# Optimization experiments

Hardware: AMD Instinct MI355X
Metric: run time of the kernel (lower is better)

The kernel has to match this reference:

```python
import jax, jax.numpy as jnp
import numpy as np

H = 8            # num_heads
WIN = 128        # num_windows (sliding-window half-width)
B, T, C = 2, 4096, 512


def setup_inputs() -> dict:
    key = jax.random.key(0)
    k1, k2, k3 = jax.random.split(key, 3)
    x = jax.random.normal(k1, (B, T, C), dtype=jnp.float32)
    W_qkv = jax.random.normal(k2, (C, 3 * C), dtype=jnp.float32) * (C ** -0.5)
    W_out = jax.random.normal(k3, (C, C), dtype=jnp.float32) * (C ** -0.5)
    b_out = jnp.zeros((C,), dtype=jnp.float32)
    return {"x": x, "W_qkv": W_qkv, "W_out": W_out, "b_out": b_out}


def reference(x, W_qkv, W_out, b_out):
    Bx, Tx, Cx = x.shape
    hd = Cx // H
    scale = hd ** -0.5
    # qkv projection -> [B, T, 3, H, hd]
    qkv = (x @ W_qkv).reshape(Bx, Tx, 3, H, hd)
    q, k, v = qkv[:, :, 0], qkv[:, :, 1], qkv[:, :, 2]  # each [B, T, H, hd]
    # attention scores [B, H, T, T]
    scores = jnp.einsum('bihd,bjhd->bhij', q, k) * scale
    idx = jnp.arange(Tx)
    band = jnp.abs(idx[:, None] - idx[None, :]) <= WIN  # [T, T] bool
    scores = jnp.where(band[None, None], scores, jnp.float32(-jnp.inf))
    attn = jax.nn.softmax(scores, axis=-1)
    # dropout is identity in eval mode (p handled by config; omitted)
    out = jnp.einsum('bhij,bjhd->bihd', attn, v).reshape(Bx, Tx, Cx)
    return out @ W_out + b_out
```

## Files before the change

kernel.cpp:

```cpp
#include <hip/hip_runtime.h>
#include <stdint.h>

typedef unsigned short ushort_t;
typedef __attribute__((ext_vector_type(8))) __bf16 bf16x8;
typedef __attribute__((ext_vector_type(8))) unsigned short ushortx8;
typedef __attribute__((ext_vector_type(4))) float floatx4;
typedef __attribute__((ext_vector_type(4))) unsigned int uint4v;

__device__ inline ushort_t f2bf(float f) {
  union { float f; unsigned u; } v; v.f = f;
  unsigned r = v.u + 0x7FFFu + ((v.u >> 16) & 1u);
  return (ushort_t)(r >> 16);
}

__device__ inline floatx4 mfma16(bf16x8 a, bf16x8 b, floatx4 c) {
  return __builtin_amdgcn_mfma_f32_16x16x32_bf16(a, b, c, 0, 0, 0);
}

__device__ inline void gload_lds16(const ushort_t* g, ushort_t* l) {
  __builtin_amdgcn_global_load_lds((__attribute__((address_space(1))) void*)(void*)(g),
                                   (__attribute__((address_space(3))) void*)(l),
                                   16, 0, 0);
}

__global__ __launch_bounds__(256)
void k_prep(const float* __restrict__ x, ushort_t* __restrict__ xb,
            const float* __restrict__ Wqkv, ushort_t* __restrict__ wqkvT,
            const float* __restrict__ Wout, ushort_t* __restrict__ woutT) {
  int bx = blockIdx.x, tid = threadIdx.x;
  if (bx < 4096) {
    int i = (bx * 256 + tid) * 4;
    float4 v = *(const float4*)(x + i);
    ushort4 o;
    o.x = f2bf(v.x); o.y = f2bf(v.y); o.z = f2bf(v.z); o.w = f2bf(v.w);
    *(ushort4*)(xb + i) = o;
    return;
  }
  __shared__ float tile[32][33];
  const float* src; ushort_t* dst; int N, id;
  if (bx < 4096 + 768) { id = bx - 4096; src = Wqkv; dst = wqkvT; N = 1536; }
  else                 { id = bx - 4864; src = Wout; dst = woutT; N = 512;  }
  int k0 = (id & 15) * 32, n0 = (id >> 4) * 32;
  int c = tid & 31, r0 = tid >> 5;
#pragma unroll
  for (int i = 0; i < 4; ++i) {
    int r = r0 + i * 8;
    tile[r][c] = src[(size_t)(k0 + r) * N + n0 + c];
  }
  __syncthreads();
#pragma unroll
  for (int i = 0; i < 4; ++i) {
    int r = r0 + i * 8;
    dst[(size_t)(n0 + r) * 512 + k0 + c] = f2bf(tile[c][r]);
  }
}

__global__ __launch_bounds__(256)
void k_gemm1(const ushort_t* __restrict__ A, const ushort_t* __restrict__ Bt,
             ushort_t* __restrict__ qd, ushort_t* __restrict__ kd,
             ushort_t* __restrict__ vtd) {
  __shared__ __align__(16) ushort_t smem[17408];
  ushort_t* As = smem;
  ushort_t* Bs = smem + 8192;
  const int tid = threadIdx.x;
  const int w = tid >> 6, l = tid & 63;
  const int lr = l & 15, lq = l >> 4;
  const int m0 = blockIdx.x * 128, n0 = blockIdx.y * 128;
  const int wm = w >> 1, wn = w & 1;

  floatx4 acc[4][4];
#pragma unroll
  for (int i = 0; i < 4; ++i)
#pragma unroll
    for (int j = 0; j < 4; ++j) acc[i][j] = (floatx4)0.0f;

  for (int k0 = 0; k0 < 512; k0 += 64) {
#pragma unroll
    for (int i = 0; i < 8; ++i) {
      int idx = w * 8 + i;
      if (idx < 16) {
        int blk = idx >> 1, half = idx & 1;
        gload_lds16(A + (size_t)(m0 + blk * 16 + lr) * 512 + k0 + half * 32 + lq * 8,
                    &As[blk * 1024 + half * 512]);
      } else {
        int j = idx - 16, blk = j >> 1, half = j & 1;
        gload_lds16(Bt + (size_t)(n0 + blk * 16 + lr) * 512 + k0 + half * 32 + lq * 8,
                    &Bs[blk * 1024 + half * 512]);
      }
    }
    __syncthreads();
#pragma unroll
    for (int half = 0; half < 2; ++half) {
      bf16x8 af[4], bfr[4];
#pragma unroll
      for (int i = 0; i < 4; ++i)
        af[i] = *(const bf16x8*)&As[(wm * 4 + i) * 1024 + half * 512 + l * 8];
#pragma unroll
      for (int j = 0; j < 4; ++j)
        bfr[j] = *(const bf16x8*)&Bs[(wn * 4 + j) * 1024 + half * 512 + l * 8];
#pragma unroll
      for (int i = 0; i < 4; ++i)
#pragma unroll
        for (int j = 0; j < 4; ++j) acc[i][j] = mfma16(af[i], bfr[j], acc[i][j]);
    }
    __syncthreads();
  }

  if (blockIdx.y < 8) {
#pragma unroll
    for (int i = 0; i < 4; ++i)
#pragma unroll
      for (int j = 0; j < 4; ++j) {
        int col = wn * 64 + j * 16 + lr;
#pragma unroll
        for (int r = 0; r < 4; ++r) {
          int row = wm * 64 + i * 16 + lq * 4 + r;
          smem[row * 136 + col] = f2bf(acc[i][j][r]);
        }
      }
    __syncthreads();
#pragma unroll
    for (int p = 0; p < 8; ++p) {
      int row = p * 16 + (tid >> 4), c8 = (tid & 15) * 8;
      ushortx8 vv = *(const ushortx8*)&smem[row * 136 + c8];
      int n = n0 + c8;
      ushort_t* dst = (n >> 9) ? kd : qd;
      int h = (n >> 6) & 7, d = n & 63;
      int m = m0 + row, b = m >> 12, t = m & 4095;
      *(ushortx8*)&dst[(((size_t)(b * 8 + h)) * 4096 + t) * 64 + d] = vv;
    }
  } else {
#pragma unroll
    for (int i = 0; i < 4; ++i)
#pragma unroll
      for (int j = 0; j < 4; ++j) {
        int dcol = wn * 64 + j * 16 + lr;
        int trow = wm * 64 + i * 16 + lq * 4;
        ushort4 pv;
        pv.x = f2bf(acc[i][j][0]); pv.y = f2bf(acc[i][j][1]);
        pv.z = f2bf(acc[i][j][2]); pv.w = f2bf(acc[i][j][3]);
        *(ushort4*)&smem[dcol * 136 + trow] = pv;
      }
    __syncthreads();
#pragma unroll
    for (int p = 0; p < 8; ++p) {
      int row = p * 16 + (tid >> 4), c8 = (tid & 15) * 8;
      ushortx8 vv = *(const ushortx8*)&smem[row * 136 + c8];
      int n = n0 + row, h = (n >> 6) & 7, d = n & 63;
      int m = m0 + c8, b = m >> 12, t = m & 4095;
      *(ushortx8*)&vtd[(((size_t)(b * 8 + h)) * 64 + d) * 4096 + t] = vv;
    }
  }
}

__global__ __launch_bounds__(256)
void k_gemm2(const ushort_t* __restrict__ A, const ushort_t* __restrict__ Bt,
             float* __restrict__ outf, const float* __restrict__ bias) {
  __shared__ __align__(16) char smemc[33792];
  ushort_t* As = (ushort_t*)smemc;
  ushort_t* Bs = (ushort_t*)(smemc + 8192);
  float* Cs = (float*)smemc;
  const int tid = threadIdx.x;
  const int w = tid >> 6, l = tid & 63;
  const int lr = l & 15, lq = l >> 4;
  const int m0 = blockIdx.x * 64, n0 = blockIdx.y * 128;
  const int wm = w >> 1, wn = w & 1;

  floatx4 acc[2][4];
#pragma unroll
  for (int i = 0; i < 2; ++i)
#pragma unroll
    for (int j = 0; j < 4; ++j) acc[i][j] = (floatx4)0.0f;

  for (int k0 = 0; k0 < 512; k0 += 64) {
#pragma unroll
    for (int i = 0; i < 6; ++i) {
      int idx = w * 6 + i;
      if (idx < 8) {
        int blk = idx >> 1, half = idx & 1;
        gload_lds16(A + (size_t)(m0 + blk * 16 + lr) * 512 + k0 + half * 32 + lq * 8,
                    &As[blk * 1024 + half * 512]);
      } else {
        int j = idx - 8, blk = j >> 1, half = j & 1;
        gload_lds16(Bt + (size_t)(n0 + blk * 16 + lr) * 512 + k0 + half * 32 + lq * 8,
                    &Bs[blk * 1024 + half * 512]);
      }
    }
    __syncthreads();
#pragma unroll
    for (int half = 0; half < 2; ++half) {
      bf16x8 af[2], bfr[4];
#pragma unroll
      for (int i = 0; i < 2; ++i)
        af[i] = *(const bf16x8*)&As[(wm * 2 + i) * 1024 + half * 512 + l * 8];
#pragma unroll
      for (int j = 0; j < 4; ++j)
        bfr[j] = *(const bf16x8*)&Bs[(wn * 4 + j) * 1024 + half * 512 + l * 8];
#pragma unroll
      for (int i = 0; i < 2; ++i)
#pragma unroll
        for (int j = 0; j < 4; ++j) acc[i][j] = mfma16(af[i], bfr[j], acc[i][j]);
    }
    __syncthreads();
  }

#pragma unroll
  for (int i = 0; i < 2; ++i)
#pragma unroll
    for (int j = 0; j < 4; ++j) {
      int col = wn * 64 + j * 16 + lr;
      float bv = bias[n0 + col];
#pragma unroll
      for (int r = 0; r < 4; ++r) {
        int row = wm * 32 + i * 16 + lq * 4 + r;
        Cs[row * 132 + col] = acc[i][j][r] + bv;
      }
    }
  __syncthreads();
#pragma unroll
  for (int p = 0; p < 4; ++p) {
    int row = p * 16 + (tid >> 4), c = (tid & 15) * 8;
    float4 v0 = *(const float4*)&Cs[row * 132 + c];
    float4 v1 = *(const float4*)&Cs[row * 132 + c + 4];
    float* op = &outf[(size_t)(m0 + row) * 512 + n0 + c];
    *(float4*)op = v0;
    *(float4*)(op + 4) = v1;
  }
}

__global__ __launch_bounds__(256)
void k_attn(const ushort_t* __restrict__ qa, const ushort_t* __restrict__ ka,
            const ushort_t* __restrict__ vta, ushort_t* __restrict__ ao) {
  __shared__ __align__(16) ushort_t S[20 * 1024];
  const int tid = threadIdx.x, w = tid >> 6, l = tid & 63;
  const int lr = l & 15, lq = l >> 4;
  const int bh = blockIdx.y, qt0 = blockIdx.x * 64;
  const int qrow = qt0 + w * 16;

  const ushort_t* kbase = ka + (size_t)bh * 4096 * 64;
#pragma unroll
  for (int i = 0; i < 10; ++i) {
    int idx = w * 10 + i, blk = idx >> 1, half = idx & 1;
    int row = qt0 - 128 + blk * 16 + lr;
    row = min(max(row, 0), 4095);
    gload_lds16(kbase + (size_t)row * 64 + half * 32 + lq * 8, &S[blk * 1024 + half * 512]);
  }

  const ushort_t* qp = qa + ((size_t)bh * 4096 + qrow + lr) * 64 + lq * 8;
  bf16x8 qf0 = *(const bf16x8*)qp;
  bf16x8 qf1 = *(const bf16x8*)(qp + 32);

  __syncthreads();

  const float Cc = 0.125f * 1.4426950408889634f;
  uint2 pk[18];
  pk[17].x = 0u; pk[17].y = 0u;
  float ps = 0.f;
#pragma unroll
  for (int kt = 0; kt < 17; ++kt) {
    const ushort_t* kp = &S[(w + kt) * 1024 + l * 8];
    bf16x8 kf0 = *(const bf16x8*)kp;
    bf16x8 kf1 = *(const bf16x8*)(kp + 512);
    floatx4 s = (floatx4)0.0f;
    s = mfma16(kf0, qf0, s);
    s = mfma16(kf1, qf1, s);
    float p[4];
#pragma unroll
    for (int r = 0; r < 4; ++r) {
      int r_rel = kt * 16 + lq * 4 + r;
      int kj = qrow - 128 + r_rel;
      bool ok = (kj >= 0) && (kj < 4096) && (r_rel >= lr) && (r_rel - lr <= 256);
      float e = ok ? exp2f(s[r] * Cc) : 0.f;
      ps += e;
      p[r] = e;
    }
    pk[kt].x = (unsigned)f2bf(p[0]) | ((unsigned)f2bf(p[1]) << 16);
    pk[kt].y = (unsigned)f2bf(p[2]) | ((unsigned)f2bf(p[3]) << 16);
  }

  ps += __shfl_xor(ps, 16, 64);
  ps += __shfl_xor(ps, 32, 64);
  float inv = __builtin_amdgcn_rcpf(ps);
  float invr[4];
#pragma unroll
  for (int r = 0; r < 4; ++r) invr[r] = __shfl(inv, lq * 4 + r, 64);

  __syncthreads();

  const ushort_t* vbase = vta + (size_t)bh * 64 * 4096;
#pragma unroll
  for (int i = 0; i < 10; ++i) {
    int t = w * 10 + i, kt2 = t >> 2, nt = t & 3;
    int d = nt * 16 + lr;
    int key = qt0 - 128 + kt2 * 32 + lq * 8;
    key = min(max(key, 0), 4088);
    gload_lds16(vbase + (size_t)d * 4096 + key, &S[t * 512]);
  }

  const int srcA = ((l >> 4) & 1) * 32 + lr;
  const int srcB = srcA + 16;
  const bool selhi = (l & 32) != 0;
  bf16x8 pu9[9];
#pragma unroll
  for (int kk = 0; kk < 9; ++kk) {
    unsigned e0 = __shfl(pk[2 * kk].x, srcA, 64);
    unsigned e1 = __shfl(pk[2 * kk].y, srcA, 64);
    unsigned e2 = __shfl(pk[2 * kk].x, srcB, 64);
    unsigned e3 = __shfl(pk[2 * kk].y, srcB, 64);
    unsigned o0 = __shfl(pk[2 * kk + 1].x, srcA, 64);
    unsigned o1 = __shfl(pk[2 * kk + 1].y, srcA, 64);
    unsigned o2 = __shfl(pk[2 * kk + 1].x, srcB, 64);
    unsigned o3 = __shfl(pk[2 * kk + 1].y, srcB, 64);
    union { uint4v u; bf16x8 b; } pu;
    pu.u[0] = selhi ? o0 : e0;
    pu.u[1] = selhi ? o1 : e1;
    pu.u[2] = selhi ? o2 : e2;
    pu.u[3] = selhi ? o3 : e3;
    pu9[kk] = pu.b;
  }

  __syncthreads();

  floatx4 oacc[4];
#pragma unroll
  for (int nt = 0; nt < 4; ++nt) oacc[nt] = (floatx4)0.0f;
#pragma unroll
  for (int kk = 0; kk < 9; ++kk) {
    int keyrel = w * 16 + kk * 32 + lq * 8;
    keyrel = min(keyrel, 312);
    int kt2 = keyrel >> 5, seg = (keyrel >> 3) & 3;
    const ushort_t* vsp = &S[kt2 * 2048 + seg * 128 + lr * 8];
#pragma unroll
    for (int nt = 0; nt < 4; ++nt) {
      bf16x8 vf = *(const bf16x8*)(vsp + nt * 512);
      oacc[nt] = mfma16(pu9[kk], vf, oacc[nt]);
    }
  }

  __syncthreads();

#pragma unroll
  for (int nt = 0; nt < 4; ++nt)
#pragma unroll
    for (int r = 0; r < 4; ++r)
      S[(w * 16 + lq * 4 + r) * 72 + nt * 16 + lr] = f2bf(oacc[nt][r] * invr[r]);
  __syncthreads();

  int b = bh >> 3, h = bh & 7;
#pragma unroll
  for (int p = 0; p < 2; ++p) {
    int row = p * 32 + (tid >> 3), c8 = (tid & 7) * 8;
    ushortx8 vv = *(const ushortx8*)&S[row * 72 + c8];
    *(ushortx8*)&ao[((size_t)(b * 4096 + qt0 + row)) * 512 + h * 64 + c8] = vv;
  }
}

extern "C" void kernel_launch(void* const* d_in, const int* in_sizes, int n_in,
                              void* d_out, int out_size, void* d_ws, size_t ws_size,
                              hipStream_t stream) {
  const float* x    = (const float*)d_in[0];
  const float* Wqkv = (const float*)d_in[1];
  const float* Wout = (const float*)d_in[2];
  const float* bout = (const float*)d_in[3];
  float* out = (float*)d_out;
  char* ws = (char*)d_ws;
  const size_t MB = 1024 * 1024;

  ushort_t* xb    = (ushort_t*)(ws);
  ushort_t* wqkvT = (ushort_t*)(ws + 8 * MB);
  ushort_t* woutT = (ushort_t*)(ws + 9 * MB + MB/2);
  ushort_t* q     = (ushort_t*)(ws + 10 * MB);
  ushort_t* k     = (ushort_t*)(ws + 18 * MB);
  ushort_t* vt    = (ushort_t*)(ws + 26 * MB);
  ushort_t* ao    = xb;

  k_prep<<<5120, 256, 0, stream>>>(x, xb, Wqkv, wqkvT, Wout, woutT);
  k_gemm1<<<dim3(64, 12), 256, 0, stream>>>(xb, wqkvT, q, k, vt);
  k_attn<<<dim3(64, 16), 256, 0, stream>>>(q, k, vt, ao);
  k_gemm2<<<dim3(128, 4), 256, 0, stream>>>(ao, woutT, out, bout);
}
```

Baseline: 143.8 us.

## Prefetch V alongside K in attention and shrink out-proj GEMM tiles

The attention kernel now issues the V loads up front together with the K tile. Half of V goes to extra LDS and the other half goes straight into registers, which removes the mid-kernel barrier and the serialized V load. Every warp now computes scores against all 20 key tiles of the block's 320-key window with an explicit band mask, instead of only its own 17 tiles. That adds some wasted MFMA and exp work but makes the indexing uniform. Separately, the output-projection GEMM moves from 64x128 to 64x64 tiles, doubling the grid for more parallelism at the cost of more A reloads and higher register/LDS pressure in attention.

```diff
diff --git a/kernel.cpp b/kernel.cpp
--- a/kernel.cpp
+++ b/kernel.cpp
@@ -156,26 +156,26 @@
 __global__ __launch_bounds__(256)
 void k_gemm2(const ushort_t* __restrict__ A, const ushort_t* __restrict__ Bt,
              float* __restrict__ outf, const float* __restrict__ bias) {
-  __shared__ __align__(16) char smemc[33792];
+  __shared__ __align__(16) char smemc[17408];
   ushort_t* As = (ushort_t*)smemc;
   ushort_t* Bs = (ushort_t*)(smemc + 8192);
   float* Cs = (float*)smemc;
   const int tid = threadIdx.x;
   const int w = tid >> 6, l = tid & 63;
   const int lr = l & 15, lq = l >> 4;
-  const int m0 = blockIdx.x * 64, n0 = blockIdx.y * 128;
+  const int m0 = blockIdx.x * 64, n0 = blockIdx.y * 64;
   const int wm = w >> 1, wn = w & 1;
 
-  floatx4 acc[2][4];
+  floatx4 acc[2][2];
 #pragma unroll
   for (int i = 0; i < 2; ++i)
 #pragma unroll
-    for (int j = 0; j < 4; ++j) acc[i][j] = (floatx4)0.0f;
+    for (int j = 0; j < 2; ++j) acc[i][j] = (floatx4)0.0f;
 
   for (int k0 = 0; k0 < 512; k0 += 64) {
 #pragma unroll
-    for (int i = 0; i < 6; ++i) {
-      int idx = w * 6 + i;
+    for (int i = 0; i < 4; ++i) {
+      int idx = w * 4 + i;
       if (idx < 8) {
         int blk = idx >> 1, half = idx & 1;
         gload_lds16(A + (size_t)(m0 + blk * 16 + lr) * 512 + k0 + half * 32 + lq * 8,
@@ -189,17 +189,17 @@
     __syncthreads();
 #pragma unroll
     for (int half = 0; half < 2; ++half) {
-      bf16x8 af[2], bfr[4];
+      bf16x8 af[2], bfr[2];
 #pragma unroll
       for (int i = 0; i < 2; ++i)
         af[i] = *(const bf16x8*)&As[(wm * 2 + i) * 1024 + half * 512 + l * 8];
 #pragma unroll
-      for (int j = 0; j < 4; ++j)
-        bfr[j] = *(const bf16x8*)&Bs[(wn * 4 + j) * 1024 + half * 512 + l * 8];
+      for (int j = 0; j < 2; ++j)
+        bfr[j] = *(const bf16x8*)&Bs[(wn * 2 + j) * 1024 + half * 512 + l * 8];
 #pragma unroll
       for (int i = 0; i < 2; ++i)
 #pragma unroll
-        for (int j = 0; j < 4; ++j) acc[i][j] = mfma16(af[i], bfr[j], acc[i][j]);
+        for (int j = 0; j < 2; ++j) acc[i][j] = mfma16(af[i], bfr[j], acc[i][j]);
     }
     __syncthreads();
   }
@@ -207,31 +207,28 @@
 #pragma unroll
   for (int i = 0; i < 2; ++i)
 #pragma unroll
-    for (int j = 0; j < 4; ++j) {
-      int col = wn * 64 + j * 16 + lr;
+    for (int j = 0; j < 2; ++j) {
+      int col = wn * 32 + j * 16 + lr;
       float bv = bias[n0 + col];
 #pragma unroll
       for (int r = 0; r < 4; ++r) {
         int row = wm * 32 + i * 16 + lq * 4 + r;
-        Cs[row * 132 + col] = acc[i][j][r] + bv;
+        Cs[row * 68 + col] = acc[i][j][r] + bv;
       }
     }
   __syncthreads();
 #pragma unroll
   for (int p = 0; p < 4; ++p) {
-    int row = p * 16 + (tid >> 4), c = (tid & 15) * 8;
-    float4 v0 = *(const float4*)&Cs[row * 132 + c];
-    float4 v1 = *(const float4*)&Cs[row * 132 + c + 4];
-    float* op = &outf[(size_t)(m0 + row) * 512 + n0 + c];
-    *(float4*)op = v0;
-    *(float4*)(op + 4) = v1;
+    int row = p * 16 + (tid >> 4), c = (tid & 15) * 4;
+    float4 v0 = *(const float4*)&Cs[row * 68 + c];
+    *(float4*)&outf[(size_t)(m0 + row) * 512 + n0 + c] = v0;
   }
 }
 
 __global__ __launch_bounds__(256)
 void k_attn(const ushort_t* __restrict__ qa, const ushort_t* __restrict__ ka,
             const ushort_t* __restrict__ vta, ushort_t* __restrict__ ao) {
-  __shared__ __align__(16) ushort_t S[20 * 1024];
+  __shared__ __align__(16) ushort_t S[30720];
   const int tid = threadIdx.x, w = tid >> 6, l = tid & 63;
   const int lr = l & 15, lq = l >> 4;
   const int bh = blockIdx.y, qt0 = blockIdx.x * 64;
@@ -245,7 +242,26 @@
     row = min(max(row, 0), 4095);
     gload_lds16(kbase + (size_t)row * 64 + half * 32 + lq * 8, &S[blk * 1024 + half * 512]);
   }
-
+  const ushort_t* vbase = vta + (size_t)bh * 64 * 4096;
+#pragma unroll
+  for (int i = 0; i < 5; ++i) {
+    int t = w * 5 + i;
+    int kt2 = t >> 2, nt = t & 3;
+    int d = nt * 16 + lr;
+    int key = qt0 - 128 + kt2 * 32 + lq * 8;
+    key = min(max(key, 0), 4088);
+    gload_lds16(vbase + (size_t)d * 4096 + key, &S[20480 + t * 512]);
+  }
+  bf16x8 vf2[5][4];
+#pragma unroll
+  for (int c = 0; c < 5; ++c)
+#pragma unroll
+    for (int nt = 0; nt < 4; ++nt) {
+      int d = nt * 16 + lr;
+      int key = qt0 - 128 + (5 + c) * 32 + lq * 8;
+      key = min(max(key, 0), 4088);
+      vf2[c][nt] = *(const bf16x8*)(vbase + (size_t)d * 4096 + key);
+    }
   const ushort_t* qp = qa + ((size_t)bh * 4096 + qrow + lr) * 64 + lq * 8;
   bf16x8 qf0 = *(const bf16x8*)qp;
   bf16x8 qf1 = *(const bf16x8*)(qp + 32);
@@ -253,12 +269,12 @@
   __syncthreads();
 
   const float Cc = 0.125f * 1.4426950408889634f;
-  uint2 pk[18];
-  pk[17].x = 0u; pk[17].y = 0u;
+  uint2 pk[20];
   float ps = 0.f;
-#pragma unroll
-  for (int kt = 0; kt < 17; ++kt) {
-    const ushort_t* kp = &S[(w + kt) * 1024 + l * 8];
+  const int q = qrow + lr;
+#pragma unroll
+  for (int bt = 0; bt < 20; ++bt) {
+    const ushort_t* kp = &S[bt * 1024 + l * 8];
     bf16x8 kf0 = *(const bf16x8*)kp;
     bf16x8 kf1 = *(const bf16x8*)(kp + 512);
     floatx4 s = (floatx4)0.0f;
@@ -267,15 +283,14 @@
     float p[4];
 #pragma unroll
     for (int r = 0; r < 4; ++r) {
-      int r_rel = kt * 16 + lq * 4 + r;
-      int kj = qrow - 128 + r_rel;
-      bool ok = (kj >= 0) && (kj < 4096) && (r_rel >= lr) && (r_rel - lr <= 256);
+      int kj = qt0 - 128 + bt * 16 + lq * 4 + r;
+      bool ok = (kj >= 0) && (kj < 4096) && (q - kj <= 128) && (kj - q <= 128);
       float e = ok ? exp2f(s[r] * Cc) : 0.f;
       ps += e;
       p[r] = e;
     }
-    pk[kt].x = (unsigned)f2bf(p[0]) | ((unsigned)f2bf(p[1]) << 16);
-    pk[kt].y = (unsigned)f2bf(p[2]) | ((unsigned)f2bf(p[3]) << 16);
+    pk[bt].x = (unsigned)f2bf(p[0]) | ((unsigned)f2bf(p[1]) << 16);
+    pk[bt].y = (unsigned)f2bf(p[2]) | ((unsigned)f2bf(p[3]) << 16);
   }
 
   ps += __shfl_xor(ps, 16, 64);
@@ -285,24 +300,12 @@
 #pragma unroll
   for (int r = 0; r < 4; ++r) invr[r] = __shfl(inv, lq * 4 + r, 64);
 
-  __syncthreads();
-
-  const ushort_t* vbase = vta + (size_t)bh * 64 * 4096;
-#pragma unroll
-  for (int i = 0; i < 10; ++i) {
-    int t = w * 10 + i, kt2 = t >> 2, nt = t & 3;
-    int d = nt * 16 + lr;
-    int key = qt0 - 128 + kt2 * 32 + lq * 8;
-    key = min(max(key, 0), 4088);
-    gload_lds16(vbase + (size_t)d * 4096 + key, &S[t * 512]);
-  }
-
   const int srcA = ((l >> 4) & 1) * 32 + lr;
   const int srcB = srcA + 16;
   const bool selhi = (l & 32) != 0;
-  bf16x8 pu9[9];
-#pragma unroll
-  for (int kk = 0; kk < 9; ++kk) {
+  bf16x8 pu[10];
+#pragma unroll
+  for (int kk = 0; kk < 10; ++kk) {
     unsigned e0 = __shfl(pk[2 * kk].x, srcA, 64);
     unsigned e1 = __shfl(pk[2 * kk].y, srcA, 64);
     unsigned e2 = __shfl(pk[2 * kk].x, srcB, 64);
@@ -311,31 +314,31 @@
     unsigned o1 = __shfl(pk[2 * kk + 1].y, srcA, 64);
     unsigned o2 = __shfl(pk[2 * kk + 1].x, srcB, 64);
     unsigned o3 = __shfl(pk[2 * kk + 1].y, srcB, 64);
-    union { uint4v u; bf16x8 b; } pu;
-    pu.u[0] = selhi ? o0 : e0;
-    pu.u[1] = selhi ? o1 : e1;
-    pu.u[2] = selhi ? o2 : e2;
-    pu.u[3] = selhi ? o3 : e3;
-    pu9[kk] = pu.b;
-  }
-
-  __syncthreads();
+    union { uint4v u; bf16x8 b; } t;
+    t.u[0] = selhi ? o0 : e0;
+    t.u[1] = selhi ? o1 : e1;
+    t.u[2] = selhi ? o2 : e2;
+    t.u[3] = selhi ? o3 : e3;
+    pu[kk] = t.b;
+  }
 
   floatx4 oacc[4];
 #pragma unroll
   for (int nt = 0; nt < 4; ++nt) oacc[nt] = (floatx4)0.0f;
 #pragma unroll
-  for (int kk = 0; kk < 9; ++kk) {
-    int keyrel = w * 16 + kk * 32 + lq * 8;
-    keyrel = min(keyrel, 312);
-    int kt2 = keyrel >> 5, seg = (keyrel >> 3) & 3;
-    const ushort_t* vsp = &S[kt2 * 2048 + seg * 128 + lr * 8];
+  for (int kk = 0; kk < 5; ++kk) {
+    const ushort_t* vsp = &S[20480 + kk * 2048 + lq * 128 + lr * 8];
 #pragma unroll
     for (int nt = 0; nt < 4; ++nt) {
       bf16x8 vf = *(const bf16x8*)(vsp + nt * 512);
-      oacc[nt] = mfma16(pu9[kk], vf, oacc[nt]);
-    }
-  }
+      oacc[nt] = mfma16(pu[kk], vf, oacc[nt]);
+    }
+  }
+#pragma unroll
+  for (int kk = 5; kk < 10; ++kk)
+#pragma unroll
+    for (int nt = 0; nt < 4; ++nt)
+      oacc[nt] = mfma16(pu[kk], vf2[kk - 5][nt], oacc[nt]);
 
   __syncthreads();
 
@@ -377,5 +380,5 @@
   k_prep<<<5120, 256, 0, stream>>>(x, xb, Wqkv, wqkvT, Wout, woutT);
   k_gemm1<<<dim3(64, 12), 256, 0, stream>>>(xb, wqkvT, q, k, vt);
   k_attn<<<dim3(64, 16), 256, 0, stream>>>(q, k, vt, ao);
-  k_gemm2<<<dim3(128, 4), 256, 0, stream>>>(ao, woutT, out, bout);
-}
+  k_gemm2<<<dim3(128, 8), 256, 0, stream>>>(ao, woutT, out, bout);
+}
```

Measured after the change: 156.1 us. 1.09x slower.
